# Kernel tuning notes

Hardware: AMD Instinct MI355X
Metric: run time of the kernel (lower is better)

The kernel has to match this reference:

```python
import jax, jax.numpy as jnp
import numpy as np

ANCESTOR_INDEX = [[], [0], [0], [0], [0, 1], [0, 2], [0, 3], [0, 1, 4], [0, 2, 5], [0, 3, 6], [0, 1, 4, 7], [0, 2, 5, 8], [0, 3, 6, 9], [0, 3, 6, 9], [0, 3, 6, 9], [0, 3, 6, 9, 12], [0, 3, 6, 9, 13], [0, 3, 6, 9, 14], [0, 3, 6, 9, 13, 16], [0, 3, 6, 9, 14, 17], [0, 3, 6, 9, 13, 16, 18], [0, 3, 6, 9, 14, 17, 19], [0, 3, 6, 9, 13, 16, 18, 20], [0, 3, 6, 9, 14, 17, 19, 21]]
HID = 1024
NP6 = 6
MAXIN = HID + NP6 * 8 + 6


def setup_inputs() -> dict:
    key = jax.random.key(0)
    ks = jax.random.split(key, 18)
    B, T = 2048, 16
    s = 0.02
    inp = {
        'x': jax.random.normal(ks[0], (B, T, 256), jnp.float32),
        'init_pose': jax.random.normal(ks[1], (B, T, 144), jnp.float32) * 0.1,
        'init_shape': jax.random.normal(ks[2], (B, T, 10), jnp.float32) * 0.1,
        'init_cam': jax.random.normal(ks[3], (B, T, 3), jnp.float32) * 0.1,
        'fc1_w': jax.random.normal(ks[4], (HID, 256 + 10), jnp.float32) * s,
        'fc1_b': jnp.zeros((HID,), jnp.float32),
        'fc2_w': jax.random.normal(ks[5], (HID, 256 + 144), jnp.float32) * s,
        'fc2_b': jnp.zeros((HID,), jnp.float32),
        'decshape_w': jax.random.normal(ks[6], (10, HID), jnp.float32) * s,
        'decshape_b': jnp.zeros((10,), jnp.float32),
        'deccam_w': jax.random.normal(ks[7], (3, 2 * HID + 3), jnp.float32) * s,
        'deccam_b': jnp.zeros((3,), jnp.float32),
        'ktd_w': jax.random.normal(ks[8], (24, NP6, MAXIN), jnp.float32) * 0.01,
        'ktd_b': jnp.zeros((24, NP6), jnp.float32),
    }
    return inp


def reference(x, init_pose, init_shape, init_cam, fc1_w, fc1_b, fc2_w, fc2_b,
              decshape_w, decshape_b, deccam_w, deccam_b, ktd_w, ktd_b):
    # fc1 / fc2 (dropout is identity in eval mode)
    xc_shape_cam = jnp.concatenate([x, init_shape], -1) @ fc1_w.T + fc1_b   # [B,T,HID]
    xc_pose_cam = jnp.concatenate([x, init_pose], -1) @ fc2_w.T + fc2_b     # [B,T,HID]

    pose = []
    for j, anc in enumerate(ANCESTOR_INDEX):
        parts = [xc_pose_cam] + [pose[i] for i in anc] + [init_pose[..., j:j + 6]]
        inp = jnp.concatenate(parts, -1)
        pad = MAXIN - inp.shape[-1]
        if pad:
            inp = jnp.pad(inp, ((0, 0), (0, 0), (0, pad)))
        pose.append(jnp.einsum('btd,od->bto', inp, ktd_w[j]) + ktd_b[j])
    pred_pose = jnp.concatenate(pose, -1) + init_pose                        # [B,T,144]

    pred_shape = xc_shape_cam @ decshape_w.T + decshape_b + init_shape      # [B,T,10]
    pred_cam = (jnp.concatenate([xc_pose_cam, xc_shape_cam, init_cam], -1)
                @ deccam_w.T + deccam_b + init_cam)                          # [B,T,3]

    pred_pose = pred_pose.reshape(-1, 144)
    pred_shape = pred_shape.reshape(-1, 10)
    pred_cam = pred_cam.reshape(-1, 3)
    # theta layout matches original output: [cam | pose | shape]
    return jnp.concatenate([pred_cam, pred_pose, pred_shape], -1)           # [B*T,157]
```

## Files before the change

### kernel.cpp

```cpp
#include <hip/hip_runtime.h>
#include <hip/hip_bf16.h>

typedef __attribute__((ext_vector_type(8))) short bf16x8;
typedef __attribute__((ext_vector_type(4))) float f32x4;

static constexpr int ALEN[24] = {0,1,1,1,2,2,2,3,3,3,4,4,4,4,4,5,5,5,6,6,7,7,8,8};
static constexpr int AOFF[24] = {0,0,1,2,3,5,7,9,12,15,18,22,26,30,34,38,43,48,53,59,65,72,79,87};
static constexpr int AFLAT[95] = {
  0, 0, 0,
  0,1, 0,2, 0,3,
  0,1,4, 0,2,5, 0,3,6,
  0,1,4,7, 0,2,5,8, 0,3,6,9, 0,3,6,9, 0,3,6,9,
  0,3,6,9,12, 0,3,6,9,13, 0,3,6,9,14,
  0,3,6,9,13,16, 0,3,6,9,14,17,
  0,3,6,9,13,16,18, 0,3,6,9,14,17,19,
  0,3,6,9,13,16,18,20, 0,3,6,9,14,17,19,21};
static constexpr int LVLN[9] = {1,3,3,3,5,3,2,2,2};
static constexpr int LVLJ[9][5] = {
  {0,0,0,0,0},{1,2,3,0,0},{4,5,6,0,0},{7,8,9,0,0},{10,11,12,13,14},
  {15,16,17,0,0},{18,19,0,0,0},{20,21,0,0,0},{22,23,0,0,0}};

static __device__ __forceinline__ unsigned short f2bf(float f) {
  unsigned int u = __float_as_uint(f);
  u = (u + 0x7fffu + ((u >> 16) & 1u)) >> 16;
  return (unsigned short)u;
}

static __device__ __forceinline__ bf16x8 pack8(float4 lo, float4 hi) {
  bf16x8 r;
  r[0] = (short)f2bf(lo.x); r[1] = (short)f2bf(lo.y);
  r[2] = (short)f2bf(lo.z); r[3] = (short)f2bf(lo.w);
  r[4] = (short)f2bf(hi.x); r[5] = (short)f2bf(hi.y);
  r[6] = (short)f2bf(hi.z); r[7] = (short)f2bf(hi.w);
  return r;
}

__global__ __launch_bounds__(256) void combine_plus(const float* __restrict__ ktd,
                                                    const float* __restrict__ dcw,
                                                    const float* __restrict__ dsw,
                                                    const float* __restrict__ w2,
                                                    const float* __restrict__ b2,
                                                    const float* __restrict__ w1,
                                                    const float* __restrict__ b1,
                                                    float* __restrict__ Gp,
                                                    float* __restrict__ Hp,
                                                    float* __restrict__ S) {
  __shared__ float shpool[5760];
  const int tid = threadIdx.x;

  if (blockIdx.y == 41) {
    if (blockIdx.x >= 4 || blockIdx.z != 0) return;
    float* Sl = shpool;
    const int c0 = blockIdx.x * 36;
    for (int lv = 0; lv < 9; lv++) {
      int units = LVLN[lv] * 54;
      for (int u = tid; u < units; u += 256) {
        int jj = u / 54, rem = u % 54, r = rem / 9, q = rem % 9;
        int j = LVLJ[lv][jj];
        int t = 6 * j + r;
        int cb = c0 + q * 4;
        f32x4 v;
        v[0] = (t == cb)     ? 1.f : 0.f;
        v[1] = (t == cb + 1) ? 1.f : 0.f;
        v[2] = (t == cb + 2) ? 1.f : 0.f;
        v[3] = (t == cb + 3) ? 1.f : 0.f;
        const float* wrow = ktd + (size_t)t * 1078 + 1024;
        for (int a = 0; a < ALEN[j]; a++) {
          int anc = AFLAT[AOFF[j] + a];
          const float* w = wrow + 6 * a;
          #pragma unroll
          for (int k = 0; k < 6; k++) {
            f32x4 s4 = *(const f32x4*)&Sl[(anc * 6 + k) * 40 + q * 4];
            float wk = w[k];
            v[0] += wk * s4[0]; v[1] += wk * s4[1];
            v[2] += wk * s4[2]; v[3] += wk * s4[3];
          }
        }
        *(f32x4*)&Sl[t * 40 + q * 4] = v;
      }
      __syncthreads();
    }
    for (int i = tid; i < 144 * 36; i += 256) {
      int t = i / 36, cc = i % 36;
      S[t * 144 + c0 + cc] = Sl[t * 40 + cc];
    }
    return;
  }

  const bool isH = blockIdx.y >= 37;
  if (isH && blockIdx.x >= 5) return;
  float (*red)[4][64] = (float(*)[4][64])shpool;
  const int w = tid >> 6, lane = tid & 63;
  const int c = blockIdx.x * 64 + lane;
  const int h0 = blockIdx.z * 128 + w * 32;

  const float* vp[4];
  int o0;
  if (!isH) {
    o0 = blockIdx.y * 4;
    #pragma unroll
    for (int oi = 0; oi < 4; oi++) {
      int o = o0 + oi; if (o > 146) o = 146;
      vp[oi] = (o < 144) ? (ktd + (size_t)o * 1078) : (dcw + (size_t)(o - 144) * 2051);
    }
  } else {
    o0 = (blockIdx.y - 37) * 4;
    #pragma unroll
    for (int oi = 0; oi < 4; oi++) {
      int o = o0 + oi; if (o > 12) o = 12;
      vp[oi] = (o < 10) ? (dsw + (size_t)o * 1024) : (dcw + (size_t)(o - 10) * 2051 + 1024);
    }
  }

  float acc[4] = {0.f, 0.f, 0.f, 0.f};
  if (!isH) {
    #pragma unroll 16
    for (int hh = 0; hh < 32; hh++) {
      int h = h0 + hh;
      float wv = (c < 400) ? w2[h * 400 + c] : ((c == 400) ? b2[h] : 0.f);
      #pragma unroll
      for (int oi = 0; oi < 4; oi++) acc[oi] += vp[oi][h] * wv;
    }
  } else {
    #pragma unroll 16
    for (int hh = 0; hh < 32; hh++) {
      int h = h0 + hh;
      float wv = (c < 266) ? w1[h * 266 + c] : ((c == 266) ? b1[h] : 0.f);
      #pragma unroll
      for (int oi = 0; oi < 4; oi++) acc[oi] += vp[oi][h] * wv;
    }
  }

  #pragma unroll
  for (int oi = 0; oi < 4; oi++) red[w][oi][lane] = acc[oi];
  __syncthreads();
  if (w == 0) {
    #pragma unroll
    for (int oi = 0; oi < 4; oi++) {
      int o = o0 + oi;
      float s = red[0][oi][lane] + red[1][oi][lane] + red[2][oi][lane] + red[3][oi][lane];
      if (!isH) {
        if (o < 147 && c <= 400) Gp[(size_t)blockIdx.z * 59200 + o * 401 + c] = s;
      } else {
        if (o < 13 && c <= 266) Hp[(size_t)blockIdx.z * 3520 + o * 267 + c] = s;
      }
    }
  }
}

static __device__ __forceinline__ float gsum(const float* __restrict__ Gp, int t, int c) {
  float s = 0.f;
  #pragma unroll
  for (int z = 0; z < 8; z++) s += Gp[(size_t)z * 59200 + t * 401 + c];
  return s;
}
static __device__ __forceinline__ float hsum(const float* __restrict__ Hp, int t, int c) {
  float s = 0.f;
  #pragma unroll
  for (int z = 0; z < 8; z++) s += Hp[(size_t)z * 3520 + t * 267 + c];
  return s;
}

__global__ __launch_bounds__(256) void assembleM(const float* __restrict__ Gp,
                                                 const float* __restrict__ Hp,
                                                 const float* __restrict__ dcw,
                                                 const float* __restrict__ dcb,
                                                 const float* __restrict__ dsb,
                                                 const float* __restrict__ ktd,
                                                 const float* __restrict__ ktdb,
                                                 float* __restrict__ M0,
                                                 float* __restrict__ C0) {
  int o = blockIdx.x;
  for (int c = threadIdx.x; c < 424; c += 256) {
    float val = 0.f;
    if (c < 413) {
      if (o < 3) {
        if (c < 400) val += gsum(Gp, 144 + o, c);
        if (c < 256) val += hsum(Hp, 10 + o, c);
        if (c >= 400 && c < 410) val += hsum(Hp, 10 + o, 256 + (c - 400));
        if (c >= 410) {
          val += dcw[(size_t)o * 2051 + 2048 + (c - 410)];
          if ((c - 410) == o) val += 1.f;
        }
      } else if (o < 147) {
        int t = o - 3, j = t / 6;
        if (c < 400) val = gsum(Gp, t, c);
        int cj = c - 256 - j;
        if (cj >= 0 && cj < 6) val += ktd[(size_t)t * 1078 + 1024 + 6 * ALEN[j] + cj];
      } else if (o < 157) {
        int s = o - 147;
        if (c < 256) val = hsum(Hp, s, c);
        if (c >= 400 && c < 410) {
          val += hsum(Hp, s, 256 + (c - 400));
          if ((c - 400) == s) val += 1.f;
        }
      }
    }
    M0[o * 424 + c] = val;
  }
  if (threadIdx.x == 0 && o < 157) {
    float bv;
    if (o < 3)        bv = gsum(Gp, 144 + o, 400) + hsum(Hp, 10 + o, 266) + dcb[o];
    else if (o < 147) bv = gsum(Gp, o - 3, 400) + ktdb[o - 3];
    else              bv = hsum(Hp, o - 147, 266) + dsb[o - 147];
    C0[o] = bv;
  }
}

__global__ __launch_bounds__(256) void foldS(const float* __restrict__ S,
                                             const float* __restrict__ M0,
                                             const float* __restrict__ C0,
                                             unsigned short* __restrict__ Mb,
                                             float* __restrict__ Cb) {
  int o = blockIdx.x;
  int c = blockIdx.y * 212 + threadIdx.x;
  bool act = (threadIdx.x < 212) && (c < 424);
  if (o < 3 || o >= 147) {
    if (act) Mb[o * 424 + c] = f2bf(M0[o * 424 + c]);
    if (threadIdx.x == 0 && blockIdx.y == 0) Cb[o] = (o < 157) ? C0[o] : 0.f;
    return;
  }
  int t = o - 3;
  __shared__ float Sl[144];
  if (threadIdx.x < 144) Sl[threadIdx.x] = S[t * 144 + threadIdx.x];
  __syncthreads();
  if (act) {
    float acc = 0.f;
    #pragma unroll 16
    for (int k = 0; k < 144; k++) acc += Sl[k] * M0[(3 + k) * 424 + c];
    if (c == 256 + t) acc += 1.f;
    Mb[o * 424 + c] = f2bf(acc);
  }
  if (threadIdx.x == 0 && blockIdx.y == 0) {
    float acc = 0.f;
    for (int k = 0; k < 144; k++) acc += Sl[k] * C0[3 + k];
    Cb[o] = acc;
  }
}

__global__ __launch_bounds__(512, 1) void main_gemm(const float* __restrict__ x,
                                                    const float* __restrict__ ipose,
                                                    const float* __restrict__ ishape,
                                                    const float* __restrict__ icam,
                                                    const unsigned short* __restrict__ Mb,
                                                    const float* __restrict__ Cb,
                                                    float* __restrict__ out) {
  __shared__ unsigned short Bl[160 * 424];
  const int tid = threadIdx.x;
  const int w = tid >> 6, lane = tid & 63;
  const int m = lane & 15, g = lane >> 4;
  const int rowbase = blockIdx.x * 128 + w * 16;
  const int row = rowbase + m;
  const float* xr = x + (size_t)row * 256;
  const float* pr = ipose + (size_t)row * 144;

  {
    const bf16x8* src = (const bf16x8*)Mb;
    bf16x8* dst = (bf16x8*)Bl;
    for (int i = tid; i < 160 * 424 / 8; i += 512) dst[i] = src[i];
  }

  float4 alo[13], ahi[13];
  #pragma unroll
  for (int k = 0; k < 8; k++) {
    const float* p = xr + k * 32 + g * 8;
    alo[k] = *(const float4*)p; ahi[k] = *(const float4*)(p + 4);
  }
  #pragma unroll
  for (int k = 8; k < 12; k++) {
    const float* p = pr + (k - 8) * 32 + g * 8;
    alo[k] = *(const float4*)p; ahi[k] = *(const float4*)(p + 4);
  }
  if (g < 2) {
    const float* p = pr + 128 + g * 8;
    alo[12] = *(const float4*)p; ahi[12] = *(const float4*)(p + 4);
  } else if (g == 2) {
    const float* p = ishape + (size_t)row * 10;
    alo[12] = make_float4(p[0], p[1], p[2], p[3]);
    ahi[12] = make_float4(p[4], p[5], p[6], p[7]);
  } else {
    const float* p = ishape + (size_t)row * 10;
    const float* q = icam + (size_t)row * 3;
    alo[12] = make_float4(p[8], p[9], q[0], q[1]);
    ahi[12] = make_float4(q[2], 0.f, 0.f, 0.f);
  }
  #pragma unroll
  for (int k = 0; k < 13; k++) {
    asm volatile("" :: "v"(alo[k].x), "v"(alo[k].y), "v"(alo[k].z), "v"(alo[k].w));
    asm volatile("" :: "v"(ahi[k].x), "v"(ahi[k].y), "v"(ahi[k].z), "v"(ahi[k].w));
  }

  __syncthreads();

  bf16x8 areg[13];
  #pragma unroll
  for (int k = 0; k < 13; k++) areg[k] = pack8(alo[k], ahi[k]);

  f32x4 acc[10];
  #pragma unroll
  for (int n = 0; n < 10; n++) acc[n] = (f32x4){0.f, 0.f, 0.f, 0.f};

  #pragma unroll
  for (int k = 0; k < 13; k++) {
    #pragma unroll
    for (int n = 0; n < 10; n++) {
      bf16x8 b = *(const bf16x8*)&Bl[(n * 16 + m) * 424 + k * 32 + g * 8];
      acc[n] = __builtin_amdgcn_mfma_f32_16x16x32_bf16(areg[k], b, acc[n], 0, 0, 0);
    }
  }

  #pragma unroll
  for (int n = 0; n < 10; n++) {
    int col = n * 16 + m;
    if (col < 157) {
      float bias = Cb[col];
      #pragma unroll
      for (int q = 0; q < 4; q++)
        out[(size_t)(rowbase + g * 4 + q) * 157 + col] = acc[n][q] + bias;
    }
  }
}

extern "C" void kernel_launch(void* const* d_in, const int* in_sizes, int n_in,
                              void* d_out, int out_size, void* d_ws, size_t ws_size,
                              hipStream_t stream) {
  const float* x      = (const float*)d_in[0];
  const float* ipose  = (const float*)d_in[1];
  const float* ishape = (const float*)d_in[2];
  const float* icam   = (const float*)d_in[3];
  const float* fc1w   = (const float*)d_in[4];
  const float* fc1b   = (const float*)d_in[5];
  const float* fc2w   = (const float*)d_in[6];
  const float* fc2b   = (const float*)d_in[7];
  const float* dsw    = (const float*)d_in[8];
  const float* dsb    = (const float*)d_in[9];
  const float* dcw    = (const float*)d_in[10];
  const float* dcb    = (const float*)d_in[11];
  const float* ktd    = (const float*)d_in[12];
  const float* ktdb   = (const float*)d_in[13];
  int rows = in_sizes[0] / 256;
  float* ws = (float*)d_ws;

  float* Gp = ws;
  float* Hp = ws + 473600;
  float* M0 = ws + 501760;
  float* C0 = ws + 569600;
  float* S  = ws + 569760;
  float* Cb = ws + 590496;
  unsigned short* Mb = (unsigned short*)(ws + 590656);

  combine_plus<<<dim3(7, 42, 8), 256, 0, stream>>>(ktd, dcw, dsw, fc2w, fc2b,
                                                   fc1w, fc1b, Gp, Hp, S);
  assembleM<<<160, 256, 0, stream>>>(Gp, Hp, dcw, dcb, dsb, ktd, ktdb, M0, C0);
  foldS<<<dim3(160, 2), 256, 0, stream>>>(S, M0, C0, Mb, Cb);
  main_gemm<<<rows / 128, 512, 0, stream>>>(x, ipose, ishape, icam, Mb, Cb,
                                            (float*)d_out);
}
```

Baseline: 60.98 us.

## Fuse assembleM and foldS into one column-tiled kernel; stage GEMM output via LDS

Merges the two weight-preparation kernels into a single launch. Each block builds a 32-column slice of M0 in shared memory, applies the S fold directly, and writes bf16 Mb, with one extra block handling the bias fold. This removes a launch and the global M0/C0 round trip. The main GEMM epilogue now writes its results into LDS and stores the 128x157 tile contiguously, giving coalesced output writes. The cost is an extra barrier and less parallelism in the fold stage (15 blocks instead of 160 and 320).

```diff
diff --git a/kernel.cpp b/kernel.cpp
--- a/kernel.cpp
+++ b/kernel.cpp
@@ -161,17 +161,46 @@
   return s;
 }
 
-__global__ __launch_bounds__(256) void assembleM(const float* __restrict__ Gp,
+__global__ __launch_bounds__(256) void fold_fuse(const float* __restrict__ Gp,
                                                  const float* __restrict__ Hp,
                                                  const float* __restrict__ dcw,
                                                  const float* __restrict__ dcb,
                                                  const float* __restrict__ dsb,
                                                  const float* __restrict__ ktd,
                                                  const float* __restrict__ ktdb,
-                                                 float* __restrict__ M0,
-                                                 float* __restrict__ C0) {
-  int o = blockIdx.x;
-  for (int c = threadIdx.x; c < 424; c += 256) {
+                                                 const float* __restrict__ S,
+                                                 unsigned short* __restrict__ Mb,
+                                                 float* __restrict__ Cb) {
+  const int tid = threadIdx.x;
+
+  if (blockIdx.x == 14) {
+    __shared__ float C0l[160];
+    if (tid < 160) {
+      int o = tid; float bv;
+      if (o < 3)        bv = gsum(Gp, 144 + o, 400) + hsum(Hp, 10 + o, 266) + dcb[o];
+      else if (o < 147) bv = gsum(Gp, o - 3, 400) + ktdb[o - 3];
+      else if (o < 157) bv = hsum(Hp, o - 147, 266) + dsb[o - 147];
+      else              bv = 0.f;
+      C0l[o] = bv;
+    }
+    __syncthreads();
+    if (tid < 3) Cb[tid] = C0l[tid];
+    else if (tid < 147) {
+      int t = tid - 3; float a = 0.f;
+      for (int k = 0; k < 144; k++) a += S[t * 144 + k] * C0l[3 + k];
+      Cb[tid] = a;
+    } else if (tid < 160) {
+      Cb[tid] = (tid < 157) ? C0l[tid] : 0.f;
+    }
+    return;
+  }
+
+  __shared__ float M0l[160][32];
+  const int c0 = blockIdx.x * 32;
+  const int cl = tid & 31;
+  const int c = c0 + cl;
+
+  for (int o = tid >> 5; o < 160; o += 8) {
     float val = 0.f;
     if (c < 413) {
       if (o < 3) {
@@ -196,45 +225,20 @@
         }
       }
     }
-    M0[o * 424 + c] = val;
-  }
-  if (threadIdx.x == 0 && o < 157) {
-    float bv;
-    if (o < 3)        bv = gsum(Gp, 144 + o, 400) + hsum(Hp, 10 + o, 266) + dcb[o];
-    else if (o < 147) bv = gsum(Gp, o - 3, 400) + ktdb[o - 3];
-    else              bv = hsum(Hp, o - 147, 266) + dsb[o - 147];
-    C0[o] = bv;
-  }
-}
-
-__global__ __launch_bounds__(256) void foldS(const float* __restrict__ S,
-                                             const float* __restrict__ M0,
-                                             const float* __restrict__ C0,
-                                             unsigned short* __restrict__ Mb,
-                                             float* __restrict__ Cb) {
-  int o = blockIdx.x;
-  int c = blockIdx.y * 212 + threadIdx.x;
-  bool act = (threadIdx.x < 212) && (c < 424);
-  if (o < 3 || o >= 147) {
-    if (act) Mb[o * 424 + c] = f2bf(M0[o * 424 + c]);
-    if (threadIdx.x == 0 && blockIdx.y == 0) Cb[o] = (o < 157) ? C0[o] : 0.f;
-    return;
-  }
-  int t = o - 3;
-  __shared__ float Sl[144];
-  if (threadIdx.x < 144) Sl[threadIdx.x] = S[t * 144 + threadIdx.x];
-  __syncthreads();
-  if (act) {
-    float acc = 0.f;
+    M0l[o][cl] = val;
+  }
+  __syncthreads();
+
+  const bool cw = (c < 424);
+  for (int o = tid >> 5; o < 160; o += 8) {
+    if ((o < 3 || o >= 147) && cw) Mb[o * 424 + c] = f2bf(M0l[o][cl]);
+  }
+  for (int t = tid >> 5; t < 144; t += 8) {
+    float a = 0.f;
     #pragma unroll 16
-    for (int k = 0; k < 144; k++) acc += Sl[k] * M0[(3 + k) * 424 + c];
-    if (c == 256 + t) acc += 1.f;
-    Mb[o * 424 + c] = f2bf(acc);
-  }
-  if (threadIdx.x == 0 && blockIdx.y == 0) {
-    float acc = 0.f;
-    for (int k = 0; k < 144; k++) acc += Sl[k] * C0[3 + k];
-    Cb[o] = acc;
+    for (int k = 0; k < 144; k++) a += S[t * 144 + k] * M0l[3 + k][cl];
+    if (c == 256 + t) a += 1.f;
+    if (cw) Mb[(3 + t) * 424 + c] = f2bf(a);
   }
 }
 
@@ -245,7 +249,7 @@
                                                     const unsigned short* __restrict__ Mb,
                                                     const float* __restrict__ Cb,
                                                     float* __restrict__ out) {
-  __shared__ unsigned short Bl[160 * 424];
+  __shared__ alignas(16) unsigned short Bl[160 * 424];
   const int tid = threadIdx.x;
   const int w = tid >> 6, lane = tid & 63;
   const int m = lane & 15, g = lane >> 4;
@@ -309,15 +313,23 @@
     }
   }
 
+  __syncthreads();
+  float* Lf = (float*)Bl;
   #pragma unroll
   for (int n = 0; n < 10; n++) {
     int col = n * 16 + m;
-    if (col < 157) {
-      float bias = Cb[col];
-      #pragma unroll
-      for (int q = 0; q < 4; q++)
-        out[(size_t)(rowbase + g * 4 + q) * 157 + col] = acc[n][q] + bias;
-    }
+    float bias = Cb[col];
+    #pragma unroll
+    for (int q = 0; q < 4; q++) {
+      int lr = w * 16 + g * 4 + q;
+      Lf[lr * 160 + col] = acc[n][q] + bias;
+    }
+  }
+  __syncthreads();
+  const size_t obase = (size_t)blockIdx.x * 128 * 157;
+  for (int i = tid; i < 128 * 157; i += 512) {
+    int r = i / 157, cc = i - r * 157;
+    out[obase + i] = Lf[r * 160 + cc];
   }
 }
 
@@ -343,16 +355,13 @@
 
   float* Gp = ws;
   float* Hp = ws + 473600;
-  float* M0 = ws + 501760;
-  float* C0 = ws + 569600;
-  float* S  = ws + 569760;
-  float* Cb = ws + 590496;
-  unsigned short* Mb = (unsigned short*)(ws + 590656);
+  float* S  = ws + 501760;
+  float* Cb = ws + 522496;
+  unsigned short* Mb = (unsigned short*)(ws + 522688);
 
   combine_plus<<<dim3(7, 42, 8), 256, 0, stream>>>(ktd, dcw, dsw, fc2w, fc2b,
                                                    fc1w, fc1b, Gp, Hp, S);
-  assembleM<<<160, 256, 0, stream>>>(Gp, Hp, dcw, dcb, dsb, ktd, ktdb, M0, C0);
-  foldS<<<dim3(160, 2), 256, 0, stream>>>(S, M0, C0, Mb, Cb);
+  fold_fuse<<<15, 256, 0, stream>>>(Gp, Hp, dcw, dcb, dsb, ktd, ktdb, S, Mb, Cb);
   main_gemm<<<rows / 128, 512, 0, stream>>>(x, ipose, ishape, icam, Mb, Cb,
                                             (float*)d_out);
 }
```

After: 109.5 us. +79.6%, slower.
